# Kernel tuning notes

Hardware: AMD Instinct MI355X
Metric: run time of the kernel (lower is better)

The kernel has to match this reference:

```python
import jax, jax.numpy as jnp
import numpy as np

B, S, D = 4, 2048, 1024

def setup_inputs() -> dict:
    key = jax.random.key(0)
    kv, kk, kq, kw = jax.random.split(key, 4)
    scale = 1.0 / np.sqrt(D)
    v = jax.random.normal(kv, (B, S, D), dtype=jnp.float32)
    k = jax.random.normal(kk, (B, S, D), dtype=jnp.float32)
    q = jax.random.normal(kq, (B, S, D), dtype=jnp.float32)
    wi = jax.random.normal(kw, (D, D), dtype=jnp.float32) * scale
    mask = jnp.tril(jnp.ones((S, S), dtype=bool))[None, :, :]  # causal [1,S,S]
    return {"v": v, "k": k, "q": q, "wi": wi, "mask": mask}

def reference(v, k, q, wi, mask):
    # project q, k, v with the shared weight wi
    q = q @ wi
    k = k @ wi
    v = v @ wi
    # scaled dot-product scores [B,S,S]
    scores = jnp.einsum('bqd,bkd->bqk', q, k) / jnp.sqrt(jnp.asarray(q.shape[-1], q.dtype))
    scores = jnp.where(mask, scores, jnp.asarray(-1e10, scores.dtype))
    attn = jax.nn.softmax(scores, axis=-1)
    # residual: q + attn @ v
    return q + jnp.einsum('bqk,bkd->bqd', attn, v)
```

## Files before the change

### kernel.cpp

```cpp
#include <hip/hip_runtime.h>
#include <hip/hip_bf16.h>

typedef __hip_bfloat16 bf16;
typedef short bf16x8 __attribute__((ext_vector_type(8)));
typedef float f32x4 __attribute__((ext_vector_type(4)));

#define HT 16384

__device__ __forceinline__ void gload16(const void* g, void* l) {
    __builtin_amdgcn_global_load_lds(
        (const __attribute__((address_space(1))) void*)g,
        (__attribute__((address_space(3))) void*)l, 16, 0, 0);
}

__device__ __forceinline__ void stage_half(char* lds, const bf16* src, int ld,
                                           int rowbase, int k0, int slotIdx,
                                           int tid)
{
    char* dst = lds + (size_t)slotIdx * HT + tid * 16;
    const int sub = tid >> 3;
    const int cb  = ((tid & 7) ^ (sub & 7)) << 4;
    #pragma unroll
    for (int p = 0; p < 2; ++p) {
        const int row = p * 64 + sub;
        const char* g = (const char*)(src + (size_t)(rowbase + row) * ld + k0) + cb;
        gload16(g, dst + p * 8192);
    }
}

__device__ __forceinline__ void stage_q(char* lds, const bf16* src, int ld,
                                        int rowbase, int k0, int slotIdx,
                                        int tid)
{
    char* dst = lds + (size_t)slotIdx * HT + tid * 16;
    #pragma unroll
    for (int p = 0; p < 4; ++p) {
        const int s = p * 256 + tid;
        const int row = s >> 3;
        const int cb = ((s & 7) ^ (row & 7)) << 4;
        const char* g = (const char*)(src + (size_t)(rowbase + row) * ld + k0) + cb;
        gload16(g, dst + p * 4096);
    }
}

__device__ __forceinline__ bf16x8 ldsfrag(const char* lds, int slotIdx,
                                          int row, int ks, int cb0)
{
    return *(const bf16x8*)(lds + (size_t)slotIdx * HT
                            + row * 128 + (cb0 ^ (ks << 6)));
}

__device__ __forceinline__ float bf2f(short s) {
    union { float f; unsigned u; } c;
    c.u = ((unsigned)(unsigned short)s) << 16;
    return c.f;
}

template<int MODE>
__launch_bounds__(512, 2)
__global__ void gemm_a256(const bf16* __restrict__ A, const bf16* __restrict__ B,
                          bf16* __restrict__ Cb, float* __restrict__ Cf)
{
    extern __shared__ char lds[];
    const int gx = gridDim.x;
    const int nwg = gx * gridDim.y;
    const int chunk = nwg >> 3;
    const int orig = blockIdx.y * gx + blockIdx.x;
    const int wk2 = (orig & 7) * chunk + (orig >> 3);
    const int bi = wk2 / gx, bj = wk2 % gx;
    const int brow = bi * 256, bcol = bj * 128;

    const int tid  = threadIdx.x;
    const int lane = tid & 63;
    const int w    = tid >> 6;
    const int wm   = w >> 1, wn = w & 1;
    const int fr   = lane & 15, fq = lane >> 4;
    const int cb0  = ((fr & 7) ^ fq) << 4;
    const int hA   = wm >> 1;
    const int rA   = (wm & 1) * 64;
    const int rB   = wn * 64;
    const int NT   = 16;

    f32x4 acc[4][4] = {};
    bf16x8 af[4][2], bv[4][2];

    stage_half(lds, A, 1024, brow,       0, 0, tid);
    stage_half(lds, A, 1024, brow + 128, 0, 1, tid);
    stage_half(lds, B, 1024, bcol,       0, 6, tid);
    stage_half(lds, A, 1024, brow,      64, 2, tid);
    stage_half(lds, A, 1024, brow + 128,64, 3, tid);
    stage_half(lds, B, 1024, bcol,     64, 7, tid);
    asm volatile("s_waitcnt vmcnt(6)" ::: "memory");
    __builtin_amdgcn_s_barrier();

#define MF8(n0)                                                               \
    _Pragma("unroll") for (int m = 0; m < 4; ++m)                             \
    _Pragma("unroll") for (int dn = 0; dn < 2; ++dn)                          \
    _Pragma("unroll") for (int ks = 0; ks < 2; ++ks)                          \
        acc[m][(n0)+dn] = __builtin_amdgcn_mfma_f32_16x16x32_bf16(            \
            af[m][ks], bv[(n0)+dn][ks], acc[m][(n0)+dn], 0, 0, 0);

    for (int t = 0; t < NT; ++t) {
        const int aslot = (t % 3) * 2 + hA;
        const int bslot = 6 + (t & 1);
        const int a2    = ((t + 2) % 3) * 2;
        const int k2    = min(t + 2, NT - 1) << 6;

        #pragma unroll
        for (int m = 0; m < 4; ++m)
            #pragma unroll
            for (int ks = 0; ks < 2; ++ks)
                af[m][ks] = ldsfrag(lds, aslot, rA + m * 16 + fr, ks, cb0);
        #pragma unroll
        for (int n = 0; n < 4; ++n)
            #pragma unroll
            for (int ks = 0; ks < 2; ++ks)
                bv[n][ks] = ldsfrag(lds, bslot, rB + n * 16 + fr, ks, cb0);
        stage_half(lds, A, 1024, brow,       k2, a2,     tid);
        stage_half(lds, A, 1024, brow + 128, k2, a2 + 1, tid);
        __builtin_amdgcn_s_barrier();
        __builtin_amdgcn_s_setprio(1);
        MF8(0)
        __builtin_amdgcn_s_setprio(0);
        __builtin_amdgcn_s_barrier();

        stage_half(lds, B, 1024, bcol, k2, bslot, tid);
        __builtin_amdgcn_s_barrier();
        __builtin_amdgcn_s_setprio(1);
        MF8(2)
        __builtin_amdgcn_s_setprio(0);
        asm volatile("s_waitcnt vmcnt(6)" ::: "memory");
        __builtin_amdgcn_s_barrier();
    }
#undef MF8

    #pragma unroll
    for (int mf = 0; mf < 4; ++mf) {
        const int r0 = brow + wm * 64 + mf * 16 + fq * 4;
        #pragma unroll
        for (int nf = 0; nf < 4; ++nf) {
            const int c = bcol + wn * 64 + nf * 16 + fr;
            #pragma unroll
            for (int j = 0; j < 4; ++j) {
                if (MODE == 0)
                    Cb[(size_t)(r0 + j) * 1024 + c] =
                        __float2bfloat16(acc[mf][nf][j]);
                else
                    Cf[(size_t)(r0 + j) * 1024 + c] = acc[mf][nf][j];
            }
        }
    }
}

template<int MODE>
__device__ __forceinline__ void tile128v2(char* lds, const bf16* A, const bf16* B,
                                          bf16* Cb, const float* Rf,
                                          int lda, int ldb, int ldcb,
                                          int brow, int bcol, int NT, float scale,
                                          int tid)
{
    const int lane = tid & 63;
    const int w    = tid >> 6;
    const int wm   = w >> 1, wn = w & 1;
    const int fr   = lane & 15, fq = lane >> 4;
    const int cb0  = ((fr & 7) ^ fq) << 4;

    f32x4 acc[4][4] = {};
    bf16x8 af[4][2], bv[4][2];

    stage_q(lds, A, lda, brow, 0,  0, tid);
    stage_q(lds, B, ldb, bcol, 0,  3, tid);
    stage_q(lds, A, lda, brow, 64, 1, tid);
    stage_q(lds, B, ldb, bcol, 64, 4, tid);
    asm volatile("s_waitcnt vmcnt(8)" ::: "memory");
    __builtin_amdgcn_s_barrier();

    for (int t = 0; t < NT; ++t) {
        const int aslot = t % 3, bslot = 3 + (t & 1);
        const int k2 = min(t + 2, NT - 1) << 6;

        #pragma unroll
        for (int m = 0; m < 4; ++m)
            #pragma unroll
            for (int ks = 0; ks < 2; ++ks)
                af[m][ks] = ldsfrag(lds, aslot, wm * 64 + m * 16 + fr, ks, cb0);
        #pragma unroll
        for (int n = 0; n < 4; ++n)
            #pragma unroll
            for (int ks = 0; ks < 2; ++ks)
                bv[n][ks] = ldsfrag(lds, bslot, wn * 64 + n * 16 + fr, ks, cb0);
        stage_q(lds, A, lda, brow, k2, (t + 2) % 3, tid);
        __builtin_amdgcn_s_barrier();
        __builtin_amdgcn_s_setprio(1);
        #pragma unroll
        for (int m = 0; m < 4; ++m)
            #pragma unroll
            for (int n = 0; n < 2; ++n)
                #pragma unroll
                for (int ks = 0; ks < 2; ++ks)
                    acc[m][n] = __builtin_amdgcn_mfma_f32_16x16x32_bf16(
                        af[m][ks], bv[n][ks], acc[m][n], 0, 0, 0);
        __builtin_amdgcn_s_setprio(0);
        __builtin_amdgcn_s_barrier();

        stage_q(lds, B, ldb, bcol, k2, bslot, tid);
        __builtin_amdgcn_s_barrier();
        __builtin_amdgcn_s_setprio(1);
        #pragma unroll
        for (int m = 0; m < 4; ++m)
            #pragma unroll
            for (int n = 2; n < 4; ++n)
                #pragma unroll
                for (int ks = 0; ks < 2; ++ks)
                    acc[m][n] = __builtin_amdgcn_mfma_f32_16x16x32_bf16(
                        af[m][ks], bv[n][ks], acc[m][n], 0, 0, 0);
        __builtin_amdgcn_s_setprio(0);
        asm volatile("s_waitcnt vmcnt(8)" ::: "memory");
        __builtin_amdgcn_s_barrier();
    }

    #pragma unroll
    for (int mf = 0; mf < 4; ++mf) {
        const int r0 = brow + wm * 64 + mf * 16 + fq * 4;
        #pragma unroll
        for (int nf = 0; nf < 4; ++nf) {
            const int c = bcol + wn * 64 + nf * 16 + fr;
            #pragma unroll
            for (int j = 0; j < 4; ++j) {
                if (MODE == 1)
                    Cb[(size_t)(r0 + j) * ldcb + c] =
                        __float2bfloat16(acc[mf][nf][j] * scale);
                else
                    Cb[(size_t)(r0 + j) * ldcb + c] = __float2bfloat16(
                        acc[mf][nf][j] + Rf[(size_t)(r0 + j) * ldcb + c]);
            }
        }
    }
}

__launch_bounds__(256, 2)
__global__ void scores128(const bf16* __restrict__ qG, const bf16* __restrict__ kb,
                          bf16* __restrict__ P)
{
    extern __shared__ char lds[];
    const int j = blockIdx.x;
    int bi = (int)((__fsqrt_rn(8.0f * j + 1.0f) - 1.0f) * 0.5f);
    while ((bi + 1) * (bi + 2) / 2 <= j) ++bi;
    while (bi * (bi + 1) / 2 > j) --bi;
    const int bj = j - bi * (bi + 1) / 2;
    const int bz = blockIdx.z;

    tile128v2<1>(lds,
                 qG + (size_t)bz * 2048 * 1024,
                 kb + (size_t)bz * 2048 * 1024,
                 P + (size_t)bz * 2048 * 2048, nullptr,
                 1024, 1024, 2048,
                 bi * 128, bj * 128, 16, 0.03125f, threadIdx.x);
}

__launch_bounds__(256, 2)
__global__ void pv128(const bf16* __restrict__ P, const bf16* __restrict__ vT,
                      const float* __restrict__ q, bf16* __restrict__ Y)
{
    extern __shared__ char lds[];
    const int x  = blockIdx.x;
    const int u  = x & 255;
    const int bs = u & 7;
    const int bj = (u >> 3) & 7;
    const int bz = u >> 6;
    const int bi = (x >> 8) ? (15 - bs) : bs;

    tile128v2<2>(lds,
                 P + (size_t)bz * 2048 * 2048,
                 vT + (size_t)bz * 1024 * 2048,
                 Y + (size_t)bz * 2048 * 1024,
                 q + (size_t)bz * 2048 * 1024,
                 2048, 2048, 1024,
                 bi * 128, bj * 128, 2 * (bi + 1), 1.0f, threadIdx.x);
}

__global__ void convert_qk_w(const float* __restrict__ q, const float* __restrict__ k,
                             const float* __restrict__ wi,
                             bf16* __restrict__ qb, bf16* __restrict__ kb,
                             bf16* __restrict__ Wb)
{
    const int N8 = 8192 * 1024 / 8;
    const int W8 = 1024 * 1024 / 8;
    const int total = 2 * N8 + W8;
    for (int i = blockIdx.x * 256 + threadIdx.x; i < total; i += gridDim.x * 256) {
        const float4* s;
        bf16* dst;
        int j;
        if (i < N8)            { s = (const float4*)q;  dst = qb; j = i; }
        else if (i < 2 * N8)   { s = (const float4*)k;  dst = kb; j = i - N8; }
        else                   { s = (const float4*)wi; dst = Wb; j = i - 2 * N8; }
        float4 a = s[2 * j], b = s[2 * j + 1];
        float vals[8] = {a.x, a.y, a.z, a.w, b.x, b.y, b.z, b.w};
        union { short h[8]; bf16x8 v8; } o;
        #pragma unroll
        for (int e = 0; e < 8; ++e) {
            bf16 hh = __float2bfloat16(vals[e]);
            o.h[e] = *(short*)&hh;
        }
        ((bf16x8*)dst)[j] = o.v8;
    }
}

__global__ void transpose_vwi(const float* __restrict__ v,
                              const float* __restrict__ wi,
                              bf16* __restrict__ vT, bf16* __restrict__ Wt)
{
    __shared__ float t[32][33];
    const int z = blockIdx.z;
    const int lx = threadIdx.x & 31, ly = threadIdx.x >> 5;
    if (z < 4) {
        const int d0 = blockIdx.x * 32, s0 = blockIdx.y * 32;
        const float* src = v + (size_t)z * 2048 * 1024;
        bf16* dst = vT + (size_t)z * 1024 * 2048;
        for (int i = ly; i < 32; i += 8)
            t[i][lx] = src[(size_t)(s0 + i) * 1024 + d0 + lx];
        __syncthreads();
        for (int i = ly; i < 32; i += 8)
            dst[(size_t)(d0 + i) * 2048 + s0 + lx] = __float2bfloat16(t[lx][i]);
    } else {
        if (blockIdx.y >= 32) return;
        const int n0 = blockIdx.x * 32, k0 = blockIdx.y * 32;
        for (int i = ly; i < 32; i += 8)
            t[i][lx] = wi[(size_t)(k0 + i) * 1024 + n0 + lx];
        __syncthreads();
        for (int i = ly; i < 32; i += 8)
            Wt[(size_t)(n0 + i) * 1024 + k0 + lx] = __float2bfloat16(t[lx][i]);
    }
}

__launch_bounds__(256)
__global__ void softmax_rows(bf16* __restrict__ P)
{
    const int wid = threadIdx.x >> 6, lane = threadIdx.x & 63;
    const int r = blockIdx.x * 4 + wid, b = blockIdx.y;
    bf16* row = P + ((size_t)b * 2048 + r) * 2048;
    const int nv  = r + 1;
    const int rup = (r & ~127) + 128;

    float vals[4][8];
    float m = -1e30f;
    #pragma unroll
    for (int c = 0; c < 4; ++c) {
        const int k0 = c * 512 + lane * 8;
        if (k0 < rup) {
            bf16x8 x = *(const bf16x8*)(row + k0);
            #pragma unroll
            for (int j = 0; j < 8; ++j) {
                float f = (k0 + j < nv) ? bf2f(x[j]) : -1e30f;
                vals[c][j] = f;
                m = fmaxf(m, f);
            }
        } else {
            #pragma unroll
            for (int j = 0; j < 8; ++j) vals[c][j] = -1e30f;
        }
    }
    #pragma unroll
    for (int o = 32; o; o >>= 1) m = fmaxf(m, __shfl_xor(m, o));

    float sum = 0.f;
    #pragma unroll
    for (int c = 0; c < 4; ++c)
        #pragma unroll
        for (int j = 0; j < 8; ++j) {
            float e = __expf(vals[c][j] - m);
            vals[c][j] = e;
            sum += e;
        }
    #pragma unroll
    for (int o = 32; o; o >>= 1) sum += __shfl_xor(sum, o);
    const float inv = 1.0f / sum;

    #pragma unroll
    for (int c = 0; c < 4; ++c) {
        const int k0 = c * 512 + lane * 8;
        if (k0 < rup) {
            union { short h[8]; bf16x8 v8; } o;
            #pragma unroll
            for (int j = 0; j < 8; ++j) {
                bf16 hh = __float2bfloat16(vals[c][j] * inv);
                o.h[j] = *(short*)&hh;
            }
            *(bf16x8*)(row + k0) = o.v8;
        }
    }
}

extern "C" void kernel_launch(void* const* d_in, const int* in_sizes, int n_in,
                              void* d_out, int out_size, void* d_ws, size_t ws_size,
                              hipStream_t stream)
{
    const float* v  = (const float*)d_in[0];
    const float* k  = (const float*)d_in[1];
    const float* q  = (const float*)d_in[2];
    const float* wi = (const float*)d_in[3];
    float* out = (float*)d_out;

    char* ws = (char*)d_ws;
    const size_t MB = 1u << 20;
    bf16* Wb = (bf16*)(ws);
    bf16* Wt = (bf16*)(ws + 2 * MB);
    bf16* G  = (bf16*)(ws + 4 * MB);
    bf16* qb = (bf16*)(ws + 6 * MB);
    bf16* kb = (bf16*)(ws + 22 * MB);
    bf16* vT = (bf16*)(ws + 38 * MB);
    bf16* qG = (bf16*)(ws + 54 * MB);
    bf16* Y  = (bf16*)(ws + 70 * MB);
    bf16* P  = (bf16*)(ws + 86 * MB);

    (void)hipFuncSetAttribute((const void*)gemm_a256<0>,
            hipFuncAttributeMaxDynamicSharedMemorySize, 131072);
    (void)hipFuncSetAttribute((const void*)gemm_a256<2>,
            hipFuncAttributeMaxDynamicSharedMemorySize, 131072);
    (void)hipFuncSetAttribute((const void*)scores128,
            hipFuncAttributeMaxDynamicSharedMemorySize, 81920);
    (void)hipFuncSetAttribute((const void*)pv128,
            hipFuncAttributeMaxDynamicSharedMemorySize, 81920);

    convert_qk_w<<<2048, 256, 0, stream>>>(q, k, wi, qb, kb, Wb);
    transpose_vwi<<<dim3(32, 64, 5), 256, 0, stream>>>(v, wi, vT, Wt);

    gemm_a256<0><<<dim3(8, 4), 512, 131072, stream>>>(Wb, Wb, G, nullptr);

    gemm_a256<0><<<dim3(8, 32), 512, 131072, stream>>>(qb, G, qG, nullptr);

    scores128<<<dim3(136, 1, 4), 256, 81920, stream>>>(qG, kb, P);

    softmax_rows<<<dim3(512, 4), 256, 0, stream>>>(P);

    pv128<<<dim3(512), 256, 81920, stream>>>(P, vT, q, Y);

    gemm_a256<2><<<dim3(8, 32), 512, 131072, stream>>>(Y, Wt, nullptr, out);
}
```

Before: 173.9 us.

## Use 256x128 tiles for causal scores GEMM and bf16 residual in PV

Replaces the 128x128 causal scores kernel with a 256x128-tile, 512-thread kernel that reuses the existing GEMM body through a macro. It enumerates 72 lower-triangular tiles per batch in an XCD-aware order, aiming for more data reuse per loaded K tile and fewer workgroups. The PV kernel now reads the residual from the bf16 copy of q instead of fp32, which halves that read traffic but loses precision. It also reorders PV block indexing so batch and row halves interleave differently. The 256-row tiles also compute more masked entries above the diagonal.

Result: no change. 176.4 us (+1.5%).

```diff
diff --git a/kernel.cpp b/kernel.cpp
--- a/kernel.cpp
+++ b/kernel.cpp
@@ -55,6 +55,51 @@
     c.u = ((unsigned)(unsigned short)s) << 16;
     return c.f;
 }
+
+#define GEMM256_BODY(A_, lda_, B_, ldb_, brow_, bcol_)                        \
+    f32x4 acc[4][4] = {};                                                     \
+    bf16x8 af[4][2], bv[4][2];                                                \
+    stage_half(lds, A_, lda_, brow_,       0, 0, tid);                        \
+    stage_half(lds, A_, lda_, brow_ + 128, 0, 1, tid);                        \
+    stage_half(lds, B_, ldb_, bcol_,       0, 6, tid);                        \
+    stage_half(lds, A_, lda_, brow_,      64, 2, tid);                        \
+    stage_half(lds, A_, lda_, brow_ + 128,64, 3, tid);                        \
+    stage_half(lds, B_, ldb_, bcol_,     64, 7, tid);                         \
+    asm volatile("s_waitcnt vmcnt(6)" ::: "memory");                          \
+    __builtin_amdgcn_s_barrier();                                             \
+    for (int t = 0; t < 16; ++t) {                                            \
+        const int aslot = (t % 3) * 2 + hA;                                   \
+        const int bslot = 6 + (t & 1);                                        \
+        const int a2    = ((t + 2) % 3) * 2;                                  \
+        const int k2    = min(t + 2, 15) << 6;                                \
+        _Pragma("unroll") for (int m = 0; m < 4; ++m)                         \
+        _Pragma("unroll") for (int ks = 0; ks < 2; ++ks)                      \
+            af[m][ks] = ldsfrag(lds, aslot, rA + m * 16 + fr, ks, cb0);       \
+        _Pragma("unroll") for (int n = 0; n < 4; ++n)                         \
+        _Pragma("unroll") for (int ks = 0; ks < 2; ++ks)                      \
+            bv[n][ks] = ldsfrag(lds, bslot, rB + n * 16 + fr, ks, cb0);       \
+        stage_half(lds, A_, lda_, brow_,       k2, a2,     tid);              \
+        stage_half(lds, A_, lda_, brow_ + 128, k2, a2 + 1, tid);              \
+        __builtin_amdgcn_s_barrier();                                         \
+        __builtin_amdgcn_s_setprio(1);                                        \
+        MF8(0)                                                                \
+        __builtin_amdgcn_s_setprio(0);                                        \
+        __builtin_amdgcn_s_barrier();                                         \
+        stage_half(lds, B_, ldb_, bcol_, k2, bslot, tid);                     \
+        __builtin_amdgcn_s_barrier();                                         \
+        __builtin_amdgcn_s_setprio(1);                                        \
+        MF8(2)                                                                \
+        __builtin_amdgcn_s_setprio(0);                                        \
+        asm volatile("s_waitcnt vmcnt(6)" ::: "memory");                      \
+        __builtin_amdgcn_s_barrier();                                         \
+    }
+
+#define MF8(n0)                                                               \
+    _Pragma("unroll") for (int m = 0; m < 4; ++m)                             \
+    _Pragma("unroll") for (int dn = 0; dn < 2; ++dn)                          \
+    _Pragma("unroll") for (int ks = 0; ks < 2; ++ks)                          \
+        acc[m][(n0)+dn] = __builtin_amdgcn_mfma_f32_16x16x32_bf16(            \
+            af[m][ks], bv[(n0)+dn][ks], acc[m][(n0)+dn], 0, 0, 0);
 
 template<int MODE>
 __launch_bounds__(512, 2)
@@ -79,60 +124,8 @@
     const int hA   = wm >> 1;
     const int rA   = (wm & 1) * 64;
     const int rB   = wn * 64;
-    const int NT   = 16;
-
-    f32x4 acc[4][4] = {};
-    bf16x8 af[4][2], bv[4][2];
-
-    stage_half(lds, A, 1024, brow,       0, 0, tid);
-    stage_half(lds, A, 1024, brow + 128, 0, 1, tid);
-    stage_half(lds, B, 1024, bcol,       0, 6, tid);
-    stage_half(lds, A, 1024, brow,      64, 2, tid);
-    stage_half(lds, A, 1024, brow + 128,64, 3, tid);
-    stage_half(lds, B, 1024, bcol,     64, 7, tid);
-    asm volatile("s_waitcnt vmcnt(6)" ::: "memory");
-    __builtin_amdgcn_s_barrier();
-
-#define MF8(n0)                                                               \
-    _Pragma("unroll") for (int m = 0; m < 4; ++m)                             \
-    _Pragma("unroll") for (int dn = 0; dn < 2; ++dn)                          \
-    _Pragma("unroll") for (int ks = 0; ks < 2; ++ks)                          \
-        acc[m][(n0)+dn] = __builtin_amdgcn_mfma_f32_16x16x32_bf16(            \
-            af[m][ks], bv[(n0)+dn][ks], acc[m][(n0)+dn], 0, 0, 0);
-
-    for (int t = 0; t < NT; ++t) {
-        const int aslot = (t % 3) * 2 + hA;
-        const int bslot = 6 + (t & 1);
-        const int a2    = ((t + 2) % 3) * 2;
-        const int k2    = min(t + 2, NT - 1) << 6;
-
-        #pragma unroll
-        for (int m = 0; m < 4; ++m)
-            #pragma unroll
-            for (int ks = 0; ks < 2; ++ks)
-                af[m][ks] = ldsfrag(lds, aslot, rA + m * 16 + fr, ks, cb0);
-        #pragma unroll
-        for (int n = 0; n < 4; ++n)
-            #pragma unroll
-            for (int ks = 0; ks < 2; ++ks)
-                bv[n][ks] = ldsfrag(lds, bslot, rB + n * 16 + fr, ks, cb0);
-        stage_half(lds, A, 1024, brow,       k2, a2,     tid);
-        stage_half(lds, A, 1024, brow + 128, k2, a2 + 1, tid);
-        __builtin_amdgcn_s_barrier();
-        __builtin_amdgcn_s_setprio(1);
-        MF8(0)
-        __builtin_amdgcn_s_setprio(0);
-        __builtin_amdgcn_s_barrier();
-
-        stage_half(lds, B, 1024, bcol, k2, bslot, tid);
-        __builtin_amdgcn_s_barrier();
-        __builtin_amdgcn_s_setprio(1);
-        MF8(2)
-        __builtin_amdgcn_s_setprio(0);
-        asm volatile("s_waitcnt vmcnt(6)" ::: "memory");
-        __builtin_amdgcn_s_barrier();
-    }
-#undef MF8
+
+    GEMM256_BODY(A, 1024, B, 1024, brow, bcol)
 
     #pragma unroll
     for (int mf = 0; mf < 4; ++mf) {
@@ -152,12 +145,55 @@
     }
 }
 
-template<int MODE>
-__device__ __forceinline__ void tile128v2(char* lds, const bf16* A, const bf16* B,
-                                          bf16* Cb, const float* Rf,
+__launch_bounds__(512, 2)
+__global__ void scores256(const bf16* __restrict__ qG, const bf16* __restrict__ kb,
+                          bf16* __restrict__ P)
+{
+    extern __shared__ char lds[];
+    const int orig = blockIdx.y * 8 + blockIdx.x;
+    const int wk2 = (orig & 7) * 36 + (orig >> 3);
+    const int bz = wk2 / 72;
+    const int j  = wk2 % 72;
+    int bi = 0;
+    #pragma unroll
+    for (int i = 1; i < 8; ++i) if (i * (i + 1) <= j) bi = i;
+    const int bj = j - bi * (bi + 1);
+    const int brow = bi * 256, bcol = bj * 128;
+
+    const bf16* A = qG + (size_t)bz * 2048 * 1024;
+    const bf16* B = kb + (size_t)bz * 2048 * 1024;
+    bf16* Cp = P + (size_t)bz * 2048 * 2048;
+
+    const int tid  = threadIdx.x;
+    const int lane = tid & 63;
+    const int w    = tid >> 6;
+    const int wm   = w >> 1, wn = w & 1;
+    const int fr   = lane & 15, fq = lane >> 4;
+    const int cb0  = ((fr & 7) ^ fq) << 4;
+    const int hA   = wm >> 1;
+    const int rA   = (wm & 1) * 64;
+    const int rB   = wn * 64;
+
+    GEMM256_BODY(A, 1024, B, 1024, brow, bcol)
+
+    #pragma unroll
+    for (int mf = 0; mf < 4; ++mf) {
+        const int r0 = brow + wm * 64 + mf * 16 + fq * 4;
+        #pragma unroll
+        for (int nf = 0; nf < 4; ++nf) {
+            const int c = bcol + wn * 64 + nf * 16 + fr;
+            #pragma unroll
+            for (int j2 = 0; j2 < 4; ++j2)
+                Cp[(size_t)(r0 + j2) * 2048 + c] =
+                    __float2bfloat16(acc[mf][nf][j2] * 0.03125f);
+        }
+    }
+}
+
+__device__ __forceinline__ void tile128pv(char* lds, const bf16* A, const bf16* B,
+                                          bf16* Cb, const bf16* Res,
                                           int lda, int ldb, int ldcb,
-                                          int brow, int bcol, int NT, float scale,
-                                          int tid)
+                                          int brow, int bcol, int NT, int tid)
 {
     const int lane = tid & 63;
     const int w    = tid >> 6;
@@ -226,57 +262,33 @@
         for (int nf = 0; nf < 4; ++nf) {
             const int c = bcol + wn * 64 + nf * 16 + fr;
             #pragma unroll
-            for (int j = 0; j < 4; ++j) {
-                if (MODE == 1)
-                    Cb[(size_t)(r0 + j) * ldcb + c] =
-                        __float2bfloat16(acc[mf][nf][j] * scale);
-                else
-                    Cb[(size_t)(r0 + j) * ldcb + c] = __float2bfloat16(
-                        acc[mf][nf][j] + Rf[(size_t)(r0 + j) * ldcb + c]);
-            }
-        }
-    }
-}
-
-__launch_bounds__(256, 2)
-__global__ void scores128(const bf16* __restrict__ qG, const bf16* __restrict__ kb,
-                          bf16* __restrict__ P)
-{
-    extern __shared__ char lds[];
-    const int j = blockIdx.x;
-    int bi = (int)((__fsqrt_rn(8.0f * j + 1.0f) - 1.0f) * 0.5f);
-    while ((bi + 1) * (bi + 2) / 2 <= j) ++bi;
-    while (bi * (bi + 1) / 2 > j) --bi;
-    const int bj = j - bi * (bi + 1) / 2;
-    const int bz = blockIdx.z;
-
-    tile128v2<1>(lds,
-                 qG + (size_t)bz * 2048 * 1024,
-                 kb + (size_t)bz * 2048 * 1024,
-                 P + (size_t)bz * 2048 * 2048, nullptr,
-                 1024, 1024, 2048,
-                 bi * 128, bj * 128, 16, 0.03125f, threadIdx.x);
+            for (int j = 0; j < 4; ++j)
+                Cb[(size_t)(r0 + j) * ldcb + c] = __float2bfloat16(
+                    acc[mf][nf][j] +
+                    __bfloat162float(Res[(size_t)(r0 + j) * ldcb + c]));
+        }
+    }
 }
 
 __launch_bounds__(256, 2)
 __global__ void pv128(const bf16* __restrict__ P, const bf16* __restrict__ vT,
-                      const float* __restrict__ q, bf16* __restrict__ Y)
+                      const bf16* __restrict__ qb, bf16* __restrict__ Y)
 {
     extern __shared__ char lds[];
-    const int x  = blockIdx.x;
-    const int u  = x & 255;
-    const int bs = u & 7;
-    const int bj = (u >> 3) & 7;
-    const int bz = u >> 6;
-    const int bi = (x >> 8) ? (15 - bs) : bs;
-
-    tile128v2<2>(lds,
-                 P + (size_t)bz * 2048 * 2048,
-                 vT + (size_t)bz * 1024 * 2048,
-                 Y + (size_t)bz * 2048 * 1024,
-                 q + (size_t)bz * 2048 * 1024,
-                 2048, 2048, 1024,
-                 bi * 128, bj * 128, 2 * (bi + 1), 1.0f, threadIdx.x);
+    const int x    = blockIdx.x;
+    const int bs   = x & 7;
+    const int half = (x >> 3) & 1;
+    const int bz   = (x >> 4) & 3;
+    const int bj   = x >> 6;
+    const int bi   = half ? (15 - bs) : bs;
+
+    tile128pv(lds,
+              P + (size_t)bz * 2048 * 2048,
+              vT + (size_t)bz * 1024 * 2048,
+              Y + (size_t)bz * 2048 * 1024,
+              qb + (size_t)bz * 2048 * 1024,
+              2048, 2048, 1024,
+              bi * 128, bj * 128, 2 * (bi + 1), threadIdx.x);
 }
 
 __global__ void convert_qk_w(const float* __restrict__ q, const float* __restrict__ k,
@@ -417,8 +429,8 @@
             hipFuncAttributeMaxDynamicSharedMemorySize, 131072);
     (void)hipFuncSetAttribute((const void*)gemm_a256<2>,
             hipFuncAttributeMaxDynamicSharedMemorySize, 131072);
-    (void)hipFuncSetAttribute((const void*)scores128,
-            hipFuncAttributeMaxDynamicSharedMemorySize, 81920);
+    (void)hipFuncSetAttribute((const void*)scores256,
+            hipFuncAttributeMaxDynamicSharedMemorySize, 131072);
     (void)hipFuncSetAttribute((const void*)pv128,
             hipFuncAttributeMaxDynamicSharedMemorySize, 81920);
 
@@ -429,11 +441,11 @@
 
     gemm_a256<0><<<dim3(8, 32), 512, 131072, stream>>>(qb, G, qG, nullptr);
 
-    scores128<<<dim3(136, 1, 4), 256, 81920, stream>>>(qG, kb, P);
+    scores256<<<dim3(8, 36), 512, 131072, stream>>>(qG, kb, P);
 
     softmax_rows<<<dim3(512, 4), 256, 0, stream>>>(P);
 
-    pv128<<<dim3(512), 256, 81920, stream>>>(P, vT, q, Y);
+    pv128<<<dim3(512), 256, 81920, stream>>>(P, vT, qb, Y);
 
     gemm_a256<2><<<dim3(8, 32), 512, 131072, stream>>>(Y, Wt, nullptr, out);
 }
```
